# Optimization experiments

Hardware: AMD Instinct MI355X
Metric: run time of the kernel (lower is better)

The kernel has to match this reference:

```python
import jax, jax.numpy as jnp
import numpy as np

# Blade metric for Cl(1,3) inner product <~A B>_0: sign per basis blade =
# (-1)^{k(k-1)/2} * prod(eta_ii) with eta = diag(1,-1,-1,-1).
# Order: 1 | e0 e1 e2 e3 | e01 e02 e03 e12 e13 e23 | e012 e013 e023 e123 | e0123
BLADE_METRIC = jnp.array(
    [1.0,
     1.0, -1.0, -1.0, -1.0,
     1.0, 1.0, 1.0, -1.0, -1.0, -1.0,
     -1.0, -1.0, -1.0, 1.0,
     -1.0],
    dtype=jnp.float32,
)

B, H, N, MVC, SC = 8, 8, 1024, 8, 32


def setup_inputs() -> dict:
    key = jax.random.key(0)
    ks = jax.random.split(key, 6)
    mv_shape = (B, H, N, MVC, 16)
    s_shape = (B, H, N, SC)
    return {
        "q_mv": jax.random.normal(ks[0], mv_shape, dtype=jnp.float32),
        "k_mv": jax.random.normal(ks[1], mv_shape, dtype=jnp.float32),
        "v_mv": jax.random.normal(ks[2], mv_shape, dtype=jnp.float32),
        "q_s": jax.random.normal(ks[3], s_shape, dtype=jnp.float32),
        "k_s": jax.random.normal(ks[4], s_shape, dtype=jnp.float32),
        "v_s": jax.random.normal(ks[5], s_shape, dtype=jnp.float32),
    }


def reference(q_mv, k_mv, v_mv, q_s, k_s, v_s):
    *lead, n_out, mvc, _ = q_mv.shape
    n_in = k_mv.shape[-3]
    sc = q_s.shape[-1]
    d = 16 * mvc + sc  # total feature dim used for the softmax scale

    # Apply GA blade metric to queries, flatten mv channels, concat scalars.
    qf = jnp.concatenate(
        [(q_mv * BLADE_METRIC).reshape(*lead, n_out, mvc * 16), q_s], axis=-1
    )
    kf = jnp.concatenate([k_mv.reshape(*lead, n_in, mvc * 16), k_s], axis=-1)
    vf = jnp.concatenate([v_mv.reshape(*lead, n_in, mvc * 16), v_s], axis=-1)

    scores = jnp.einsum("bhid,bhjd->bhij", qf, kf) / jnp.sqrt(
        jnp.asarray(d, dtype=qf.dtype)
    )
    attn = jax.nn.softmax(scores, axis=-1)
    out = jnp.einsum("bhij,bhjd->bhid", attn, vf)

    out_mv = out[..., : mvc * 16].reshape(*lead, n_out, mvc, 16)
    out_s = out[..., mvc * 16 :]
    return out_mv, out_s
```

## Files before the change

### kernel.cpp

```cpp
#include <hip/hip_runtime.h>

typedef __attribute__((ext_vector_type(8))) _Float16 f16x8;
typedef __attribute__((ext_vector_type(16))) float f32x16;

#define BHn 64
#define Nn 1024

static constexpr int kOutMvElems = 8 * 8 * 1024 * 128;
static constexpr float kScaleLog2e = 0.11405506f;
static constexpr unsigned kNegMask = 0xBF1Cu;
static constexpr int kBlob = 20480;

typedef __attribute__((address_space(1))) const void* gas1_t;
typedef __attribute__((address_space(3))) void* las3_t;
__device__ __forceinline__ void dma16(const _Float16* g, _Float16* l) {
  __builtin_amdgcn_global_load_lds((gas1_t)g, (las3_t)l, 16, 0, 0);
}
__device__ __forceinline__ float fast_exp2(float x) {
  float r;
  asm("v_exp_f32 %0, %1" : "=v"(r) : "v"(x));
  return r;
}

__global__ __launch_bounds__(256) void pack_kernel(const float* __restrict__ kmv,
                                                   const float* __restrict__ ks,
                                                   const float* __restrict__ vmv,
                                                   const float* __restrict__ vs,
                                                   _Float16* __restrict__ KV) {
  __shared__ _Float16 tk[64][184];
  __shared__ _Float16 tv[160][72];
  const int kt = blockIdx.x;
  const int bh = blockIdx.y;
  const int tid = threadIdx.x;
#pragma unroll
  for (int i = 0; i < 5; ++i) {
    int s = tid + 256 * i;
    int key = s / 20, p = s - key * 20;
    int row = bh * Nn + kt * 64 + key;
    const float* src = (p < 16) ? (kmv + (size_t)row * 128 + p * 8)
                                : (ks + (size_t)row * 32 + (p - 16) * 8);
    float4 a = *(const float4*)src;
    float4 b = *(const float4*)(src + 4);
    f16x8 h;
    h[0] = (_Float16)a.x; h[1] = (_Float16)a.y; h[2] = (_Float16)a.z; h[3] = (_Float16)a.w;
    h[4] = (_Float16)b.x; h[5] = (_Float16)b.y; h[6] = (_Float16)b.z; h[7] = (_Float16)b.w;
    *(f16x8*)&tk[key][p * 8] = h;
  }
  for (int s = tid; s < 64 * 40; s += 256) {
    int key = s / 40, p = s - key * 40;
    int row = bh * Nn + kt * 64 + key;
    const float* src = (p < 32) ? (vmv + (size_t)row * 128 + p * 4)
                                : (vs + (size_t)row * 32 + (p - 32) * 4);
    float4 v = *(const float4*)src;
    int d = p * 4;
    tv[d + 0][key] = (_Float16)v.x;
    tv[d + 1][key] = (_Float16)v.y;
    tv[d + 2][key] = (_Float16)v.z;
    tv[d + 3][key] = (_Float16)v.w;
  }
  __syncthreads();
  _Float16* dst = KV + ((size_t)bh * 16 + kt) * kBlob;
#pragma unroll
  for (int i = 0; i < 5; ++i) {
    int u = tid + 256 * i;
    int p = u >> 6, key = u & 63;
    f16x8 h = *(const f16x8*)&tk[key][p * 8];
    *(f16x8*)&dst[p * 512 + key * 8] = h;
  }
#pragma unroll
  for (int i = 0; i < 5; ++i) {
    int u = tid + 256 * i;
    int dcol = u & 31;
    int rest = u >> 5;
    int dt = rest % 5;
    int s8 = rest / 5;
    int kb = (s8 >> 1) * 16 + (s8 & 1) * 4;
    int d = 32 * dt + dcol;
    f16x8 h;
#pragma unroll
    for (int i2 = 0; i2 < 8; ++i2)
      h[i2] = tv[d][kb + (i2 & 3) + ((i2 >> 2) << 3)];
    *(f16x8*)&dst[10240 + u * 8] = h;
  }
}

__global__ __launch_bounds__(512, 1) void geo_attn_kernel(const float* __restrict__ qmv,
                                                          const float* __restrict__ qs,
                                                          const _Float16* __restrict__ KV,
                                                          float* __restrict__ out) {
  __shared__ __align__(16) _Float16 kv[3 * kBlob];

  const int b = blockIdx.x;
  const int sw = (b & 7) * 32 + (b >> 3);
  const int qb = sw & 3;
  const int bh = sw >> 2;

  const int tid = threadIdx.x;
  const int w = tid >> 6;
  const int l = tid & 63;
  const int h = l >> 5;
  const int dcol = l & 31;

  const _Float16* blob0 = KV + (size_t)bh * 16 * kBlob;

  const int kb0 = h * 512 + dcol * 8;
  const int vb0 = 10240 + h * 1280 + dcol * 8;

  const int row0w = bh * Nn + qb * 256 + w * 32;
  const size_t qrow = (size_t)(row0w + dcol);
  f16x8 qf2[10];
#pragma unroll
  for (int c = 0; c < 10; ++c) {
    const float* src = (c < 8) ? (qmv + qrow * 128 + c * 16 + 8 * h)
                               : (qs + qrow * 32 + (c - 8) * 16 + 8 * h);
    float4 a = *(const float4*)src;
    float4 b4 = *(const float4*)(src + 4);
    float x[8] = {a.x, a.y, a.z, a.w, b4.x, b4.y, b4.z, b4.w};
#pragma unroll
    for (int i = 0; i < 8; ++i) {
      float v = x[i] * kScaleLog2e;
      if (c < 8) {
        int idx = 8 * h + i;
        v = ((kNegMask >> idx) & 1u) ? -v : v;
      }
      qf2[c][i] = (_Float16)v;
    }
  }

  f32x16 acc2[5];
#pragma unroll
  for (int dt = 0; dt < 5; ++dt)
#pragma unroll
    for (int r = 0; r < 16; ++r) acc2[dt][r] = 0.f;
  float Ma = 12.f, La = 0.f;

  f32x16 s2[2];
  f16x8 pfr[4];

  const int laneOff = l * 8 + w * 512;
  auto stage = [&](int t, int buf) {
    const _Float16* src = blob0 + (size_t)t * kBlob + laneOff;
    _Float16* dst = &kv[buf * kBlob + w * 512];
#pragma unroll
    for (int i = 0; i < 5; ++i) dma16(src + i * 4096, dst + i * 4096);
  };

  auto do_qk = [&](const _Float16* blob) {
#pragma unroll
    for (int r = 0; r < 16; ++r) { s2[0][r] = 0.f; s2[1][r] = 0.f; }
    f16x8 kw[3][2];
#pragma unroll
    for (int c = 0; c < 2; ++c)
#pragma unroll
      for (int kt = 0; kt < 2; ++kt)
        kw[c][kt] = *(const f16x8*)&blob[kb0 + c * 1024 + kt * 256];
#pragma unroll
    for (int c = 0; c < 10; ++c) {
      if (c + 2 < 10) {
#pragma unroll
        for (int kt = 0; kt < 2; ++kt)
          kw[(c + 2) % 3][kt] = *(const f16x8*)&blob[kb0 + (c + 2) * 1024 + kt * 256];
      }
      s2[0] = __builtin_amdgcn_mfma_f32_32x32x16_f16(kw[c % 3][0], qf2[c], s2[0], 0, 0, 0);
      s2[1] = __builtin_amdgcn_mfma_f32_32x32x16_f16(kw[c % 3][1], qf2[c], s2[1], 0, 0, 0);
    }
  };
  auto do_pv = [&](const _Float16* blob) {
    f16x8 vf[4];
#pragma unroll
    for (int i = 0; i < 4; ++i)
      vf[i] = *(const f16x8*)&blob[vb0 + (i / 5) * 2560 + (i % 5) * 256];
#pragma unroll
    for (int i = 0; i < 20; ++i) {
      f16x8 cu = vf[i & 3];
      if (i + 4 < 20)
        vf[i & 3] = *(const f16x8*)&blob[vb0 + ((i + 4) / 5) * 2560 + ((i + 4) % 5) * 256];
      const int kc = i / 5, dt = i % 5;
      acc2[dt] = __builtin_amdgcn_mfma_f32_32x32x16_f16(pfr[kc], cu, acc2[dt], 0, 0, 0);
    }
  };
  auto do_softmax = [&]() {
    float rs = 0.f;
#pragma unroll
    for (int kt = 0; kt < 2; ++kt)
#pragma unroll
      for (int r = 0; r < 16; ++r) {
        float p_ = fast_exp2(s2[kt][r] - Ma);
        rs += p_;
        pfr[2 * kt + (r >> 3)][r & 7] = (_Float16)p_;
      }
    if (__builtin_expect(__any((int)(rs > 3.2e4f)), 0)) {
      float lm = s2[0][0];
#pragma unroll
      for (int kt = 0; kt < 2; ++kt)
#pragma unroll
        for (int r = 0; r < 16; ++r) lm = fmaxf(lm, s2[kt][r]);
      lm = fmaxf(lm, __shfl_xor(lm, 32));
      float nM = fmaxf(Ma, lm);
      float fs = fast_exp2(Ma - nM);
      Ma = nM;
      La *= fs;
#pragma unroll
      for (int r = 0; r < 16; ++r) {
        int q = (r & 3) + 8 * (r >> 2) + 4 * h;
        float fr = __shfl(fs, q, 32);
#pragma unroll
        for (int dt = 0; dt < 5; ++dt) acc2[dt][r] *= fr;
      }
      rs = 0.f;
#pragma unroll
      for (int kt = 0; kt < 2; ++kt)
#pragma unroll
        for (int r = 0; r < 16; ++r) {
          float p_ = fast_exp2(s2[kt][r] - Ma);
          rs += p_;
          pfr[2 * kt + (r >> 3)][r & 7] = (_Float16)p_;
        }
    }
    La += rs;
  };

  stage(0, 0);
  stage(1, 1);

  for (int t = 0; t < 16; ++t) {
    if (t == 15) asm volatile("s_waitcnt vmcnt(0)" ::: "memory");
    else         asm volatile("s_waitcnt vmcnt(5)" ::: "memory");
    __builtin_amdgcn_s_barrier();
    __builtin_amdgcn_sched_barrier(0);
    if (t + 2 < 16) stage(t + 2, (t + 2) % 3);
    const _Float16* blob = &kv[(t % 3) * kBlob];
    __builtin_amdgcn_s_setprio(1);
    do_qk(blob);
    __builtin_amdgcn_s_setprio(0);
    do_softmax();
    __builtin_amdgcn_s_setprio(1);
    do_pv(blob);
    __builtin_amdgcn_s_setprio(0);
  }

  La += __shfl_xor(La, 32);
  float ri = 1.f / La;
#pragma unroll
  for (int r = 0; r < 16; ++r) {
    const int q = (r & 3) + 8 * (r >> 2) + 4 * h;
    float ra = __shfl(ri, q, 32);
    const size_t orow = (size_t)(row0w + q);
#pragma unroll
    for (int dt = 0; dt < 5; ++dt) {
      float v = acc2[dt][r] * ra;
      if (dt < 4)
        out[orow * 128 + 32 * dt + dcol] = v;
      else
        out[(size_t)kOutMvElems + orow * 32 + dcol] = v;
    }
  }
}

extern "C" void kernel_launch(void* const* d_in, const int* in_sizes, int n_in,
                              void* d_out, int out_size, void* d_ws, size_t ws_size,
                              hipStream_t stream) {
  const float* qmv = (const float*)d_in[0];
  const float* kmv = (const float*)d_in[1];
  const float* vmv = (const float*)d_in[2];
  const float* qs = (const float*)d_in[3];
  const float* ks = (const float*)d_in[4];
  const float* vs = (const float*)d_in[5];
  float* out = (float*)d_out;

  _Float16* KV = (_Float16*)d_ws;

  pack_kernel<<<dim3(16, BHn), dim3(256), 0, stream>>>(kmv, ks, vmv, vs, KV);
  geo_attn_kernel<<<dim3(256), dim3(512), 0, stream>>>(qmv, qs, KV, out);
}
```

Baseline: 78.36 us.

## Read K/V fragments directly from global memory instead of LDS triple-buffer

Removes the global_load_lds triple-buffered LDS staging and the per-tile barriers, so each wave loads its K and V fragments straight from global memory (L2/L1). Launch bounds are raised to allow two blocks per CU, since LDS is no longer used. This removes the barrier synchronisation and the LDS footprint. In exchange, every wave fetches its own copy of the K/V tiles from cache, and load latency now sits directly in front of the MFMA chains with no asynchronous prefetch.

```diff
diff --git a/kernel.cpp b/kernel.cpp
--- a/kernel.cpp
+++ b/kernel.cpp
@@ -11,11 +11,6 @@
 static constexpr unsigned kNegMask = 0xBF1Cu;
 static constexpr int kBlob = 20480;
 
-typedef __attribute__((address_space(1))) const void* gas1_t;
-typedef __attribute__((address_space(3))) void* las3_t;
-__device__ __forceinline__ void dma16(const _Float16* g, _Float16* l) {
-  __builtin_amdgcn_global_load_lds((gas1_t)g, (las3_t)l, 16, 0, 0);
-}
 __device__ __forceinline__ float fast_exp2(float x) {
   float r;
   asm("v_exp_f32 %0, %1" : "=v"(r) : "v"(x));
@@ -84,12 +79,10 @@
   }
 }
 
-__global__ __launch_bounds__(512, 1) void geo_attn_kernel(const float* __restrict__ qmv,
+__global__ __launch_bounds__(512, 2) void geo_attn_kernel(const float* __restrict__ qmv,
                                                           const float* __restrict__ qs,
                                                           const _Float16* __restrict__ KV,
                                                           float* __restrict__ out) {
-  __shared__ __align__(16) _Float16 kv[3 * kBlob];
-
   const int b = blockIdx.x;
   const int sw = (b & 7) * 32 + (b >> 3);
   const int qb = sw & 3;
@@ -137,15 +130,7 @@
   f32x16 s2[2];
   f16x8 pfr[4];
 
-  const int laneOff = l * 8 + w * 512;
-  auto stage = [&](int t, int buf) {
-    const _Float16* src = blob0 + (size_t)t * kBlob + laneOff;
-    _Float16* dst = &kv[buf * kBlob + w * 512];
-#pragma unroll
-    for (int i = 0; i < 5; ++i) dma16(src + i * 4096, dst + i * 4096);
-  };
-
-  auto do_qk = [&](const _Float16* blob) {
+  auto do_qk = [&](const _Float16* gk) {
 #pragma unroll
     for (int r = 0; r < 16; ++r) { s2[0][r] = 0.f; s2[1][r] = 0.f; }
     f16x8 kw[3][2];
@@ -153,28 +138,28 @@
     for (int c = 0; c < 2; ++c)
 #pragma unroll
       for (int kt = 0; kt < 2; ++kt)
-        kw[c][kt] = *(const f16x8*)&blob[kb0 + c * 1024 + kt * 256];
+        kw[c][kt] = *(const f16x8*)&gk[kb0 + c * 1024 + kt * 256];
 #pragma unroll
     for (int c = 0; c < 10; ++c) {
       if (c + 2 < 10) {
 #pragma unroll
         for (int kt = 0; kt < 2; ++kt)
-          kw[(c + 2) % 3][kt] = *(const f16x8*)&blob[kb0 + (c + 2) * 1024 + kt * 256];
+          kw[(c + 2) % 3][kt] = *(const f16x8*)&gk[kb0 + (c + 2) * 1024 + kt * 256];
       }
       s2[0] = __builtin_amdgcn_mfma_f32_32x32x16_f16(kw[c % 3][0], qf2[c], s2[0], 0, 0, 0);
       s2[1] = __builtin_amdgcn_mfma_f32_32x32x16_f16(kw[c % 3][1], qf2[c], s2[1], 0, 0, 0);
     }
   };
-  auto do_pv = [&](const _Float16* blob) {
+  auto do_pv = [&](const _Float16* gb) {
     f16x8 vf[4];
 #pragma unroll
     for (int i = 0; i < 4; ++i)
-      vf[i] = *(const f16x8*)&blob[vb0 + (i / 5) * 2560 + (i % 5) * 256];
+      vf[i] = *(const f16x8*)&gb[vb0 + (i / 5) * 2560 + (i % 5) * 256];
 #pragma unroll
     for (int i = 0; i < 20; ++i) {
       f16x8 cu = vf[i & 3];
       if (i + 4 < 20)
-        vf[i & 3] = *(const f16x8*)&blob[vb0 + ((i + 4) / 5) * 2560 + ((i + 4) % 5) * 256];
+        vf[i & 3] = *(const f16x8*)&gb[vb0 + ((i + 4) / 5) * 2560 + ((i + 4) % 5) * 256];
       const int kc = i / 5, dt = i % 5;
       acc2[dt] = __builtin_amdgcn_mfma_f32_32x32x16_f16(pfr[kc], cu, acc2[dt], 0, 0, 0);
     }
@@ -220,22 +205,14 @@
     La += rs;
   };
 
-  stage(0, 0);
-  stage(1, 1);
-
   for (int t = 0; t < 16; ++t) {
-    if (t == 15) asm volatile("s_waitcnt vmcnt(0)" ::: "memory");
-    else         asm volatile("s_waitcnt vmcnt(5)" ::: "memory");
-    __builtin_amdgcn_s_barrier();
-    __builtin_amdgcn_sched_barrier(0);
-    if (t + 2 < 16) stage(t + 2, (t + 2) % 3);
-    const _Float16* blob = &kv[(t % 3) * kBlob];
+    const _Float16* gb = blob0 + (size_t)t * kBlob;
     __builtin_amdgcn_s_setprio(1);
-    do_qk(blob);
+    do_qk(gb);
     __builtin_amdgcn_s_setprio(0);
     do_softmax();
     __builtin_amdgcn_s_setprio(1);
-    do_pv(blob);
+    do_pv(gb);
     __builtin_amdgcn_s_setprio(0);
   }
 
```

Result: slower. 121.2 us (+54.6%).
